# Optimization experiments

Measured on AMD Instinct MI355X. Metric: run time of the kernel, lower is better.

The kernel has to match this reference:

```python
import jax, jax.numpy as jnp
import numpy as np

B, L, D = 4096, 128, 60  # states, padded buffer length, word+char+tag dim
HIDDEN, OUT = 200, 3


def setup_inputs() -> dict:
    key = jax.random.key(0)
    ks = jax.random.split(key, 8)
    buffer = jax.random.normal(ks[0], (B, L, D), dtype=jnp.float32)
    # buffer_index in [1, L-4] so buffer_index+3 stays in range (shift still legal region varies)
    buffer_index = jax.random.randint(ks[1], (B,), 0, 124)
    stack_indexes = jax.random.randint(ks[2], (B, 3), 0, L)
    stack_len = jax.random.randint(ks[3], (B,), 0, 12)
    W1 = jax.random.normal(ks[4], (6 * D, HIDDEN), dtype=jnp.float32) * 0.05
    b1 = jnp.zeros((HIDDEN,), dtype=jnp.float32)
    W2 = jax.random.normal(ks[5], (HIDDEN, OUT), dtype=jnp.float32) * 0.05
    b2 = jnp.zeros((OUT,), dtype=jnp.float32)
    return {"buffer": buffer, "W1": W1, "b1": b1, "W2": W2, "b2": b2,
            "buffer_index": buffer_index, "stack_indexes": stack_indexes,
            "stack_len": stack_len}


def reference(buffer, W1, b1, W2, b2, buffer_index, stack_indexes, stack_len):
    Bn, Ln, Dn = buffer.shape
    # gather 3 contiguous buffer slots per state: buffer[b, bi:bi+3]
    buf_idx = buffer_index[:, None] + jnp.arange(3)           # [B, 3]
    buffers = jnp.take_along_axis(buffer, buf_idx[:, :, None], axis=1).reshape(Bn, -1)
    # gather top-3 stack slots per state
    stacks = jnp.take_along_axis(buffer, stack_indexes[:, :, None], axis=1).reshape(Bn, -1)
    X = jnp.concatenate([buffers, stacks], axis=1)            # [B, 6*D]
    hid = jax.nn.relu(X @ W1 + b1)
    out = hid @ W2 + b2                                       # [B, 3]
    # legal action mask
    legal = jnp.stack([
        jnp.where(buffer_index + 3 >= Ln, 0.0, 1.0),  # shift legal iff buffer not exhausted
        jnp.where(stack_len <= 3, 0.0, 1.0),          # left-arc
        jnp.where(stack_len <= 4, 0.0, 1.0),          # right-arc
    ], axis=1).astype(jnp.float32)
    return out, legal
```

## Files before the change

### kernel.cpp

```cpp
#include <hip/hip_runtime.h>


#define Bq    4096
#define Lq    128
#define Dq    60
#define HIDq  200
#define ONUM  3
#define KTN   12
#define MB    16
#define NTHR  512
#define SLABW 196

typedef short bf16x8 __attribute__((ext_vector_type(8)));
typedef float f32x4  __attribute__((ext_vector_type(4)));

__device__ __forceinline__ unsigned int rhu(float f) {
    union { float f; unsigned int u; } x; x.f = f;
    return x.u + 0x8000u;
}
__device__ __forceinline__ unsigned pack2(float lo, float hi) {
    return __builtin_amdgcn_perm(rhu(hi), rhu(lo), 0x07060302u);
}

__device__ __forceinline__ void keep4(const float4& v) {
    asm volatile("" :: "v"(v.x), "v"(v.y), "v"(v.z), "v"(v.w));
}

__global__ __launch_bounds__(NTHR, 1) void parser_fused(
    const float* __restrict__ buffer,
    const float* __restrict__ W1,
    const float* __restrict__ b1,
    const float* __restrict__ W2,
    const float* __restrict__ b2,
    const int*   __restrict__ buffer_index,
    const int*   __restrict__ stack_indexes,
    const int*   __restrict__ stack_len,
    float*       __restrict__ out)
{
    __shared__ unsigned short Afrag[KTN * 64 * 8];
    __shared__ unsigned int   wbuf[8][16 * SLABW];
    __shared__ float          psum[8][MB][ONUM];

    const int t  = threadIdx.x;
    const int w  = t >> 6;
    const int l  = t & 63;
    const int s0 = blockIdx.x * MB;
    const bool hasB1 = (w < 5);

    int g_s[3], g_k0[3], g_seg[3], g_ri[3];
    bool g_ok[3];
    #pragma unroll
    for (int m = 0; m < 3; ++m) {
        int i = t + m * 512;
        g_ok[m] = (m < 2) || (t < 416);
        if (g_ok[m]) {
            int s = i / 90, r = i % 90, seg = r / 15, f = r % 15;
            g_s[m] = s; g_seg[m] = seg; g_k0[m] = seg * 60 + f * 4;
            g_ri[m] = (seg < 3) ? buffer_index[s0 + s]
                                : stack_indexes[(s0 + s) * 3 + (seg - 3)];
        } else { g_s[m] = 0; g_seg[m] = 0; g_k0[m] = 0; g_ri[m] = 0; }
    }

    float4 sa[12], sb[12];
    #pragma unroll
    for (int it = 0; it < 12; ++it) {
        int j = it * 64 + l;
        if (it < 11 || l < 16) {
            int k2 = j >> 2, nq = j & 3;
            int nb = w * 16 + nq * 4;
            const float* p = W1 + (size_t)(2 * k2) * HIDq + nb;
            sa[it] = *(const float4*)p;
            sb[it] = *(const float4*)(p + HIDq);
        } else {
            sa[it] = (float4){0.f, 0.f, 0.f, 0.f};
            sb[it] = (float4){0.f, 0.f, 0.f, 0.f};
        }
    }

    float4 gv[3];
    #pragma unroll
    for (int m = 0; m < 3; ++m) {
        if (g_ok[m]) {
            int row = (g_seg[m] < 3) ? (g_ri[m] + g_seg[m]) : g_ri[m];
            int off = g_k0[m] % 60;
            gv[m] = *(const float4*)(buffer +
                     ((size_t)(s0 + g_s[m]) * Lq + row) * Dq + off);
        } else {
            gv[m] = (float4){0.f, 0.f, 0.f, 0.f};
        }
    }

    #pragma unroll
    for (int it = 0; it < 12; ++it) { keep4(sa[it]); keep4(sb[it]); }

    #pragma unroll
    for (int z = 0; z < 3; ++z) {
        int idx = z * 64 + l;
        wbuf[w][(idx / 12) * SLABW + 180 + (idx % 12)] = 0u;
    }

    #pragma unroll
    for (int it = 0; it < 12; ++it) {
        int j = it * 64 + l;
        if (it < 11 || l < 16) {
            int k2 = j >> 2, nq = j & 3;
            wbuf[w][(nq * 4 + 0) * SLABW + k2] = pack2(sa[it].x, sb[it].x);
            wbuf[w][(nq * 4 + 1) * SLABW + k2] = pack2(sa[it].y, sb[it].y);
            wbuf[w][(nq * 4 + 2) * SLABW + k2] = pack2(sa[it].z, sb[it].z);
            wbuf[w][(nq * 4 + 3) * SLABW + k2] = pack2(sa[it].w, sb[it].w);
        }
    }

    float4 ta[12], tb[12];
    if (hasB1) {
        #pragma unroll
        for (int it = 0; it < 12; ++it) {
            int j = it * 64 + l;
            if (it < 11 || l < 16) {
                int k2 = j >> 2, nq = j & 3;
                int nb = 128 + w * 16 + nq * 4;
                if (nb < HIDq) {
                    const float* p = W1 + (size_t)(2 * k2) * HIDq + nb;
                    ta[it] = *(const float4*)p;
                    tb[it] = *(const float4*)(p + HIDq);
                } else {
                    ta[it] = (float4){0.f, 0.f, 0.f, 0.f};
                    tb[it] = (float4){0.f, 0.f, 0.f, 0.f};
                }
            }
        }
    }

    const int  n0   = w * 16 + (l & 15);
    const int  n1   = (8 + w) * 16 + (l & 15);
    const bool n1ok = n1 < HIDq;
    float bb0 = b1[n0];
    float w20 = W2[n0 * ONUM + 0], w21 = W2[n0 * ONUM + 1], w22 = W2[n0 * ONUM + 2];
    float bb1 = 0.f, w23 = 0.f, w24 = 0.f, w25 = 0.f;
    if (hasB1 && n1ok) {
        bb1 = b1[n1];
        w23 = W2[n1 * ONUM + 0]; w24 = W2[n1 * ONUM + 1]; w25 = W2[n1 * ONUM + 2];
    }

    bf16x8 B0[KTN], B1[KTN];
    #pragma unroll
    for (int kt = 0; kt < KTN; ++kt)
        B0[kt] = *((const bf16x8*)&wbuf[w][(l & 15) * SLABW + kt * 16 + ((l >> 4) << 2)]);

    #pragma unroll
    for (int m = 0; m < 3; ++m) {
        if (g_ok[m]) {
            int kt   = g_k0[m] >> 5;
            int lane = g_s[m] + (((g_k0[m] & 31) >> 3) << 4);
            uint2 pk;
            pk.x = pack2(gv[m].x, gv[m].y);
            pk.y = pack2(gv[m].z, gv[m].w);
            *((uint2*)&Afrag[(size_t)(kt * 64 + lane) * 8 + (g_k0[m] & 7)]) = pk;
        }
    }
    if (t < 48) {
        f32x4 z = {0.f, 0.f, 0.f, 0.f};
        *((f32x4*)&Afrag[(size_t)(11 * 64 + 16 + t) * 8]) = z;
    }
    if (t < MB * ONUM) {
        int s = t / ONUM, o = t % ONUM;
        int bi = buffer_index[s0 + s];
        int sl = stack_len[s0 + s];
        float lg;
        if (o == 0)      lg = (bi + 3 >= Lq) ? 0.f : 1.f;
        else if (o == 1) lg = (sl <= 3)      ? 0.f : 1.f;
        else             lg = (sl <= 4)      ? 0.f : 1.f;
        out[(size_t)Bq * ONUM + (size_t)(s0 + s) * ONUM + o] = lg;
    }

    if (hasB1) {
        #pragma unroll
        for (int it = 0; it < 12; ++it) { keep4(ta[it]); keep4(tb[it]); }
    }

    if (hasB1) {
        #pragma unroll
        for (int it = 0; it < 12; ++it) {
            int j = it * 64 + l;
            if (it < 11 || l < 16) {
                int k2 = j >> 2, nq = j & 3;
                wbuf[w][(nq * 4 + 0) * SLABW + k2] = pack2(ta[it].x, tb[it].x);
                wbuf[w][(nq * 4 + 1) * SLABW + k2] = pack2(ta[it].y, tb[it].y);
                wbuf[w][(nq * 4 + 2) * SLABW + k2] = pack2(ta[it].z, tb[it].z);
                wbuf[w][(nq * 4 + 3) * SLABW + k2] = pack2(ta[it].w, tb[it].w);
            }
        }
        #pragma unroll
        for (int kt = 0; kt < KTN; ++kt)
            B1[kt] = *((const bf16x8*)&wbuf[w][(l & 15) * SLABW + kt * 16 + ((l >> 4) << 2)]);
    }

    __syncthreads();

    f32x4 acc0 = {}, acc1 = {};
    #pragma unroll
    for (int kt = 0; kt < KTN; ++kt) {
        bf16x8 a = *((const bf16x8*)&Afrag[(size_t)(kt * 64 + l) * 8]);
        acc0 = __builtin_amdgcn_mfma_f32_16x16x32_bf16(a, B0[kt], acc0, 0, 0, 0);
        if (hasB1)
            acc1 = __builtin_amdgcn_mfma_f32_16x16x32_bf16(a, B1[kt], acc1, 0, 0, 0);
    }

    float p[ONUM][4];
    #pragma unroll
    for (int o = 0; o < ONUM; ++o)
        #pragma unroll
        for (int r = 0; r < 4; ++r) p[o][r] = 0.f;

    #pragma unroll
    for (int r = 0; r < 4; ++r) {
        float h = acc0[r] + bb0; h = h > 0.f ? h : 0.f;
        p[0][r] = fmaf(h, w20, p[0][r]);
        p[1][r] = fmaf(h, w21, p[1][r]);
        p[2][r] = fmaf(h, w22, p[2][r]);
    }
    if (hasB1) {
        #pragma unroll
        for (int r = 0; r < 4; ++r) {
            float h = acc1[r] + bb1; h = h > 0.f ? h : 0.f;
            p[0][r] = fmaf(h, w23, p[0][r]);
            p[1][r] = fmaf(h, w24, p[1][r]);
            p[2][r] = fmaf(h, w25, p[2][r]);
        }
    }

    #pragma unroll
    for (int d = 1; d < 16; d <<= 1) {
        #pragma unroll
        for (int o = 0; o < ONUM; ++o)
            #pragma unroll
            for (int r = 0; r < 4; ++r)
                p[o][r] += __shfl_xor(p[o][r], d, 64);
    }
    if ((l & 15) == 0) {
        #pragma unroll
        for (int r = 0; r < 4; ++r) {
            int s = ((l >> 4) << 2) + r;
            #pragma unroll
            for (int o = 0; o < ONUM; ++o) psum[w][s][o] = p[o][r];
        }
    }
    __syncthreads();

    if (t < MB * ONUM) {
        int s = t / ONUM, o = t % ONUM;
        float v = b2[o];
        #pragma unroll
        for (int w8 = 0; w8 < 8; ++w8) v += psum[w8][s][o];
        out[(size_t)(s0 + s) * ONUM + o] = v;
    }
}

extern "C" void kernel_launch(void* const* d_in, const int* in_sizes, int n_in,
                              void* d_out, int out_size, void* d_ws, size_t ws_size,
                              hipStream_t stream) {
    const float* buffer        = (const float*)d_in[0];
    const float* W1            = (const float*)d_in[1];
    const float* b1            = (const float*)d_in[2];
    const float* W2            = (const float*)d_in[3];
    const float* b2            = (const float*)d_in[4];
    const int*   buffer_index  = (const int*)d_in[5];
    const int*   stack_indexes = (const int*)d_in[6];
    const int*   stack_len     = (const int*)d_in[7];
    float*       out           = (float*)d_out;

    parser_fused<<<Bq / MB, NTHR, 0, stream>>>(
        buffer, W1, b1, W2, b2, buffer_index, stack_indexes, stack_len, out);
}
```

Measured before the change: 16.13 us.

## Stage full W1 in shared slab cooperatively and read B fragments inside MFMA loop

Replaces the per-wave W1 staging, where each wave loaded and packed only its own 16-column slabs in two phases, with a block-wide cooperative load. All 512 threads convert the whole 200x180 packed-bf16 W1 into one shared array in two k-halves. B fragments are now read from LDS inside the MFMA loop rather than preloaded into registers, with masking for padded k and out-of-range columns. This spreads global load work evenly across threads and cuts register pressure, at the cost of a larger LDS footprint (about 144KB) and extra LDS reads in the inner loop.

Result: slower. 19.79 us (+22.7%).

```diff
diff --git a/kernel.cpp b/kernel.cpp
--- a/kernel.cpp
+++ b/kernel.cpp
@@ -9,7 +9,7 @@
 #define KTN   12
 #define MB    16
 #define NTHR  512
-#define SLABW 196
+#define SLABW 180
 
 typedef short bf16x8 __attribute__((ext_vector_type(8)));
 typedef float f32x4  __attribute__((ext_vector_type(4)));
@@ -25,6 +25,8 @@
 __device__ __forceinline__ void keep4(const float4& v) {
     asm volatile("" :: "v"(v.x), "v"(v.y), "v"(v.z), "v"(v.w));
 }
+
+union BU { bf16x8 v; unsigned u[4]; };
 
 __global__ __launch_bounds__(NTHR, 1) void parser_fused(
     const float* __restrict__ buffer,
@@ -37,8 +39,8 @@
     const int*   __restrict__ stack_len,
     float*       __restrict__ out)
 {
+    __shared__ unsigned       wbuf[HIDq * SLABW];
     __shared__ unsigned short Afrag[KTN * 64 * 8];
-    __shared__ unsigned int   wbuf[8][16 * SLABW];
     __shared__ float          psum[8][MB][ONUM];
 
     const int t  = threadIdx.x;
@@ -61,19 +63,19 @@
         } else { g_s[m] = 0; g_seg[m] = 0; g_k0[m] = 0; g_ri[m] = 0; }
     }
 
-    float4 sa[12], sb[12];
-    #pragma unroll
-    for (int it = 0; it < 12; ++it) {
-        int j = it * 64 + l;
-        if (it < 11 || l < 16) {
-            int k2 = j >> 2, nq = j & 3;
-            int nb = w * 16 + nq * 4;
-            const float* p = W1 + (size_t)(2 * k2) * HIDq + nb;
-            sa[it] = *(const float4*)p;
-            sb[it] = *(const float4*)(p + HIDq);
+    float4 sa[9], sb[9];
+    #pragma unroll
+    for (int r = 0; r < 9; ++r) {
+        int j = r * 512 + t;
+        bool live = (r < 8) || (t < 404);
+        if (live) {
+            int cg = j / 90, k2 = j - cg * 90;
+            const float* p = W1 + (size_t)(2 * k2) * HIDq + cg * 4;
+            sa[r] = *(const float4*)p;
+            sb[r] = *(const float4*)(p + HIDq);
         } else {
-            sa[it] = (float4){0.f, 0.f, 0.f, 0.f};
-            sb[it] = (float4){0.f, 0.f, 0.f, 0.f};
+            sa[r] = (float4){0.f, 0.f, 0.f, 0.f};
+            sb[r] = (float4){0.f, 0.f, 0.f, 0.f};
         }
     }
 
@@ -87,47 +89,6 @@
                      ((size_t)(s0 + g_s[m]) * Lq + row) * Dq + off);
         } else {
             gv[m] = (float4){0.f, 0.f, 0.f, 0.f};
-        }
-    }
-
-    #pragma unroll
-    for (int it = 0; it < 12; ++it) { keep4(sa[it]); keep4(sb[it]); }
-
-    #pragma unroll
-    for (int z = 0; z < 3; ++z) {
-        int idx = z * 64 + l;
-        wbuf[w][(idx / 12) * SLABW + 180 + (idx % 12)] = 0u;
-    }
-
-    #pragma unroll
-    for (int it = 0; it < 12; ++it) {
-        int j = it * 64 + l;
-        if (it < 11 || l < 16) {
-            int k2 = j >> 2, nq = j & 3;
-            wbuf[w][(nq * 4 + 0) * SLABW + k2] = pack2(sa[it].x, sb[it].x);
-            wbuf[w][(nq * 4 + 1) * SLABW + k2] = pack2(sa[it].y, sb[it].y);
-            wbuf[w][(nq * 4 + 2) * SLABW + k2] = pack2(sa[it].z, sb[it].z);
-            wbuf[w][(nq * 4 + 3) * SLABW + k2] = pack2(sa[it].w, sb[it].w);
-        }
-    }
-
-    float4 ta[12], tb[12];
-    if (hasB1) {
-        #pragma unroll
-        for (int it = 0; it < 12; ++it) {
-            int j = it * 64 + l;
-            if (it < 11 || l < 16) {
-                int k2 = j >> 2, nq = j & 3;
-                int nb = 128 + w * 16 + nq * 4;
-                if (nb < HIDq) {
-                    const float* p = W1 + (size_t)(2 * k2) * HIDq + nb;
-                    ta[it] = *(const float4*)p;
-                    tb[it] = *(const float4*)(p + HIDq);
-                } else {
-                    ta[it] = (float4){0.f, 0.f, 0.f, 0.f};
-                    tb[it] = (float4){0.f, 0.f, 0.f, 0.f};
-                }
-            }
         }
     }
 
@@ -142,10 +103,37 @@
         w23 = W2[n1 * ONUM + 0]; w24 = W2[n1 * ONUM + 1]; w25 = W2[n1 * ONUM + 2];
     }
 
-    bf16x8 B0[KTN], B1[KTN];
-    #pragma unroll
-    for (int kt = 0; kt < KTN; ++kt)
-        B0[kt] = *((const bf16x8*)&wbuf[w][(l & 15) * SLABW + kt * 16 + ((l >> 4) << 2)]);
+    #pragma unroll
+    for (int r = 0; r < 9; ++r) { keep4(sa[r]); keep4(sb[r]); }
+
+    #pragma unroll
+    for (int r = 0; r < 9; ++r) {
+        int j = r * 512 + t;
+        if ((r < 8) || (t < 404)) {
+            int cg = j / 90, k2 = j - cg * 90;
+            int base = (cg * 4) * SLABW + k2;
+            wbuf[base            ] = pack2(sa[r].x, sb[r].x);
+            wbuf[base +     SLABW] = pack2(sa[r].y, sb[r].y);
+            wbuf[base + 2 * SLABW] = pack2(sa[r].z, sb[r].z);
+            wbuf[base + 3 * SLABW] = pack2(sa[r].w, sb[r].w);
+        }
+    }
+
+    float4 ta[9], tb[9];
+    #pragma unroll
+    for (int r = 0; r < 9; ++r) {
+        int j = r * 512 + t;
+        bool live = (r < 8) || (t < 404);
+        if (live) {
+            int cg = j / 90, k2 = (j - cg * 90) + 90;
+            const float* p = W1 + (size_t)(2 * k2) * HIDq + cg * 4;
+            ta[r] = *(const float4*)p;
+            tb[r] = *(const float4*)(p + HIDq);
+        } else {
+            ta[r] = (float4){0.f, 0.f, 0.f, 0.f};
+            tb[r] = (float4){0.f, 0.f, 0.f, 0.f};
+        }
+    }
 
     #pragma unroll
     for (int m = 0; m < 3; ++m) {
@@ -173,37 +161,41 @@
         out[(size_t)Bq * ONUM + (size_t)(s0 + s) * ONUM + o] = lg;
     }
 
-    if (hasB1) {
-        #pragma unroll
-        for (int it = 0; it < 12; ++it) { keep4(ta[it]); keep4(tb[it]); }
-    }
-
-    if (hasB1) {
-        #pragma unroll
-        for (int it = 0; it < 12; ++it) {
-            int j = it * 64 + l;
-            if (it < 11 || l < 16) {
-                int k2 = j >> 2, nq = j & 3;
-                wbuf[w][(nq * 4 + 0) * SLABW + k2] = pack2(ta[it].x, tb[it].x);
-                wbuf[w][(nq * 4 + 1) * SLABW + k2] = pack2(ta[it].y, tb[it].y);
-                wbuf[w][(nq * 4 + 2) * SLABW + k2] = pack2(ta[it].z, tb[it].z);
-                wbuf[w][(nq * 4 + 3) * SLABW + k2] = pack2(ta[it].w, tb[it].w);
-            }
-        }
-        #pragma unroll
-        for (int kt = 0; kt < KTN; ++kt)
-            B1[kt] = *((const bf16x8*)&wbuf[w][(l & 15) * SLABW + kt * 16 + ((l >> 4) << 2)]);
+    #pragma unroll
+    for (int r = 0; r < 9; ++r) { keep4(ta[r]); keep4(tb[r]); }
+    #pragma unroll
+    for (int r = 0; r < 9; ++r) {
+        int j = r * 512 + t;
+        if ((r < 8) || (t < 404)) {
+            int cg = j / 90, k2 = j - cg * 90;
+            int base = (cg * 4) * SLABW + k2 + 90;
+            wbuf[base            ] = pack2(ta[r].x, tb[r].x);
+            wbuf[base +     SLABW] = pack2(ta[r].y, tb[r].y);
+            wbuf[base + 2 * SLABW] = pack2(ta[r].z, tb[r].z);
+            wbuf[base + 3 * SLABW] = pack2(ta[r].w, tb[r].w);
+        }
     }
 
     __syncthreads();
 
+    const unsigned mOK = n1ok ? 0xFFFFFFFFu : 0u;
+    const int koffl = ((l >> 4) << 2);
     f32x4 acc0 = {}, acc1 = {};
     #pragma unroll
     for (int kt = 0; kt < KTN; ++kt) {
         bf16x8 a = *((const bf16x8*)&Afrag[(size_t)(kt * 64 + l) * 8]);
-        acc0 = __builtin_amdgcn_mfma_f32_16x16x32_bf16(a, B0[kt], acc0, 0, 0, 0);
-        if (hasB1)
-            acc1 = __builtin_amdgcn_mfma_f32_16x16x32_bf16(a, B1[kt], acc1, 0, 0, 0);
+        BU b0;
+        b0.v = *((const bf16x8*)&wbuf[n0 * SLABW + kt * 16 + koffl]);
+        if (kt == 11 && l >= 16) { b0.u[0] = 0; b0.u[1] = 0; b0.u[2] = 0; b0.u[3] = 0; }
+        acc0 = __builtin_amdgcn_mfma_f32_16x16x32_bf16(a, b0.v, acc0, 0, 0, 0);
+        if (hasB1) {
+            BU b1v;
+            int colB = n1ok ? n1 : 199;
+            b1v.v = *((const bf16x8*)&wbuf[colB * SLABW + kt * 16 + koffl]);
+            b1v.u[0] &= mOK; b1v.u[1] &= mOK; b1v.u[2] &= mOK; b1v.u[3] &= mOK;
+            if (kt == 11 && l >= 16) { b1v.u[0] = 0; b1v.u[1] = 0; b1v.u[2] = 0; b1v.u[3] = 0; }
+            acc1 = __builtin_amdgcn_mfma_f32_16x16x32_bf16(a, b1v.v, acc1, 0, 0, 0);
+        }
     }
 
     float p[ONUM][4];
```
